# Kernel optimization log

Measured on AMD Instinct MI355X. Metric: run time of the kernel, lower is better.

## Reference

```python
import jax, jax.numpy as jnp
import numpy as np

N = 50000       # nodes
E = 800000      # edges (before self-loops)
F_IN = 256      # input feature dim
HID = 32        # hidden per head
HEADS = 4
CLASSES = 32


def setup_inputs() -> dict:
    key = jax.random.key(0)
    ks = jax.random.split(key, 10)
    x = jax.random.normal(ks[0], (N, F_IN), dtype=jnp.float32)
    edge_index = jax.random.randint(ks[1], (2, E), 0, N, dtype=jnp.int32)
    s1 = 1.0 / np.sqrt(F_IN)
    s2 = 1.0 / np.sqrt(HEADS * HID)
    W1 = jax.random.normal(ks[2], (HEADS * HID, F_IN), dtype=jnp.float32) * s1
    a_src1 = jax.random.normal(ks[3], (HEADS, HID), dtype=jnp.float32) * 0.1
    a_dst1 = jax.random.normal(ks[4], (HEADS, HID), dtype=jnp.float32) * 0.1
    b1 = jnp.zeros((HEADS * HID,), dtype=jnp.float32)
    W2 = jax.random.normal(ks[5], (CLASSES, HEADS * HID), dtype=jnp.float32) * s2
    a_src2 = jax.random.normal(ks[6], (1, CLASSES), dtype=jnp.float32) * 0.1
    a_dst2 = jax.random.normal(ks[7], (1, CLASSES), dtype=jnp.float32) * 0.1
    b2 = jnp.zeros((CLASSES,), dtype=jnp.float32)
    return {"x": x, "edge_index": edge_index,
            "W1": W1, "a_src1": a_src1, "a_dst1": a_dst1, "b1": b1,
            "W2": W2, "a_src2": a_src2, "a_dst2": a_dst2, "b2": b2}


def gat_conv(x, src, dst, W, a_src, a_dst, b, heads, ch):
    """PyG GATConv: linear -> per-head additive attention -> segment softmax over dst -> scatter-sum."""
    n = x.shape[0]
    h = (x @ W.T).reshape(n, heads, ch)                      # [N,H,C]
    asc = jnp.einsum('nhc,hc->nh', h, a_src)                 # att_src . h_j
    adc = jnp.einsum('nhc,hc->nh', h, a_dst)                 # att_dst . h_i
    e = jax.nn.leaky_relu(asc[src] + adc[dst], 0.2)          # [E,H]
    m = jax.ops.segment_max(e, dst, num_segments=n)          # stable softmax per destination
    p = jnp.exp(e - m[dst])
    denom = jax.ops.segment_sum(p, dst, num_segments=n)
    alpha = p / (denom[dst] + 1e-16)                         # [E,H]
    out = jax.ops.segment_sum(h[src] * alpha[:, :, None], dst, num_segments=n)  # [N,H,C]
    return out.reshape(n, heads * ch) + b


def reference(x, edge_index, W1, a_src1, a_dst1, b1, W2, a_src2, a_dst2, b2):
    # PyG GATConv default add_self_loops=True
    loops = jnp.arange(N, dtype=edge_index.dtype)
    src = jnp.concatenate([edge_index[0], loops])
    dst = jnp.concatenate([edge_index[1], loops])
    h = gat_conv(x, src, dst, W1, a_src1, a_dst1, b1, HEADS, HID)
    h = jax.nn.relu(h)                                       # dropout is identity in eval mode
    out = gat_conv(h, src, dst, W2, a_src2, a_dst2, b2, 1, CLASSES)
    return jax.nn.log_softmax(out, axis=1)
```

## Files before the change

kernel.cpp:

```cpp
#include <hip/hip_runtime.h>
#include <hip/hip_fp16.h>

#define N_NODES 50000
#define E_EDGES 800000
#define ET (E_EDGES + N_NODES)
#define NBKT 1024
#define BCAP 2048
#define SCAP 2112
#define CSTR 16
#define G1_BLOCKS 391
#define P_BLOCKS 250
#define P_EPB 3200

typedef _Float16 h8 __attribute__((ext_vector_type(8)));
typedef float f32x16 __attribute__((ext_vector_type(16)));

__device__ __forceinline__ float lrelu(float v) { return v > 0.f ? v : 0.2f * v; }

__global__ __launch_bounds__(256) void prep_kernel(const float* __restrict__ W1,
                                                   const float* __restrict__ W2,
                                                   const float* __restrict__ as1,
                                                   const float* __restrict__ ad1,
                                                   _Float16* __restrict__ w1h,
                                                   _Float16* __restrict__ w2h,
                                                   int* __restrict__ cursor) {
    int i = blockIdx.x * 256 + threadIdx.x;
    if (i < NBKT * CSTR) {
        cursor[i] = 0;
    } else if (i < NBKT * CSTR + 4096) {
        int j = (i - NBKT * CSTR) * 8;
#pragma unroll
        for (int t = 0; t < 8; t++) w1h[j + t] = (_Float16)W1[j + t];
    } else if (i < NBKT * CSTR + 4608) {
        int j = (i - (NBKT * CSTR + 4096)) * 8;
#pragma unroll
        for (int t = 0; t < 8; t++) w2h[j + t] = (_Float16)W2[j + t];
    } else if (i < NBKT * CSTR + 5376) {
        int j = (i - (NBKT * CSTR + 4608)) * 8;
#pragma unroll
        for (int t = 0; t < 8; t++) w1h[136 * 256 + j + t] = (_Float16)0.f;
    } else if (i < NBKT * CSTR + 7424) {
        int a = i - (NBKT * CSTR + 5376);
        int h = a >> 8, k = a & 255;
        const float* av = (h < 4 ? as1 : ad1) + (h & 3) * 32;
        const float* wb = W1 + (size_t)(h & 3) * 32 * 256 + k;
        float s = 0.f;
#pragma unroll
        for (int c = 0; c < 32; c++) s += av[c] * wb[(size_t)c * 256];
        w1h[(size_t)(128 + h) * 256 + k] = (_Float16)s;
    }
}

__global__ __launch_bounds__(256) void gp_kernel(const float* __restrict__ x,
                                                 const int* __restrict__ ei,
                                                 const _Float16* __restrict__ w1h,
                                                 _Float16* __restrict__ h1h,
                                                 float* __restrict__ asc1,
                                                 float* __restrict__ adc1,
                                                 int* __restrict__ cursor,
                                                 int* __restrict__ scratch) {
    __shared__ int hcnt[NBKT];
    __shared__ int hbase[NBKT];
    int tid = threadIdx.x;
    if (blockIdx.x >= G1_BLOCKS) {
        int b = blockIdx.x - G1_BLOCKS;
#pragma unroll
        for (int u = 0; u < NBKT / 256; u++) hcnt[u * 256 + tid] = 0;
        __syncthreads();
        int e0 = b * P_EPB;
        const int4* s4 = (const int4*)(ei + e0);
        const int4* d4 = (const int4*)(ei + E_EDGES + e0);
        for (int q = tid; q < P_EPB / 4; q += 256) {
            int4 d = d4[q];
            atomicAdd(&hcnt[d.x >> 6], 1);
            atomicAdd(&hcnt[d.y >> 6], 1);
            atomicAdd(&hcnt[d.z >> 6], 1);
            atomicAdd(&hcnt[d.w >> 6], 1);
        }
        __syncthreads();
        int rot = (b * 197) & (NBKT - 1);
#pragma unroll
        for (int u = 0; u < NBKT / 256; u++) {
            int bb = (u * 256 + tid + rot) & (NBKT - 1);
            int c = hcnt[bb];
            hbase[bb] = (c > 0) ? atomicAdd(&cursor[bb * CSTR], c) : 0;
            hcnt[bb] = 0;
        }
        __syncthreads();
        for (int q = tid; q < P_EPB / 4; q += 256) {
            int4 s = s4[q];
            int4 d = d4[q];
            int bk, pos;
            bk = d.x >> 6; pos = hbase[bk] + atomicAdd(&hcnt[bk], 1);
            scratch[(size_t)bk * BCAP + pos] = s.x | ((d.x & 63) << 16);
            bk = d.y >> 6; pos = hbase[bk] + atomicAdd(&hcnt[bk], 1);
            scratch[(size_t)bk * BCAP + pos] = s.y | ((d.y & 63) << 16);
            bk = d.z >> 6; pos = hbase[bk] + atomicAdd(&hcnt[bk], 1);
            scratch[(size_t)bk * BCAP + pos] = s.z | ((d.z & 63) << 16);
            bk = d.w >> 6; pos = hbase[bk] + atomicAdd(&hcnt[bk], 1);
            scratch[(size_t)bk * BCAP + pos] = s.w | ((d.w & 63) << 16);
        }
        return;
    }
    int wid = tid >> 6, lane = tid & 63;
    int rbase = blockIdx.x * 128 + wid * 32;
    if (rbase >= N_NODES) return;
    int l31 = lane & 31, l5 = lane >> 5;
    int ar = rbase + l31;
    if (ar > N_NODES - 1) ar = N_NODES - 1;
    const float* ap = x + (size_t)ar * 256 + l5 * 8;
    const _Float16* bp = w1h + (size_t)l31 * 256 + l5 * 8;
    f32x16 acc0 = {}, acc1 = {}, acc2 = {}, acc3 = {}, acc4 = {};
#pragma unroll 4
    for (int ks = 0; ks < 16; ks++) {
        float4 xa = *(const float4*)(ap + ks * 16);
        float4 xb = *(const float4*)(ap + ks * 16 + 4);
        h8 av;
        av[0] = (_Float16)xa.x; av[1] = (_Float16)xa.y;
        av[2] = (_Float16)xa.z; av[3] = (_Float16)xa.w;
        av[4] = (_Float16)xb.x; av[5] = (_Float16)xb.y;
        av[6] = (_Float16)xb.z; av[7] = (_Float16)xb.w;
        h8 b0 = *(const h8*)(bp + ks * 16);
        h8 b1 = *(const h8*)(bp + 32 * 256 + ks * 16);
        h8 b2 = *(const h8*)(bp + 64 * 256 + ks * 16);
        h8 b3 = *(const h8*)(bp + 96 * 256 + ks * 16);
        h8 b4 = *(const h8*)(bp + 128 * 256 + ks * 16);
        acc0 = __builtin_amdgcn_mfma_f32_32x32x16_f16(av, b0, acc0, 0, 0, 0);
        acc1 = __builtin_amdgcn_mfma_f32_32x32x16_f16(av, b1, acc1, 0, 0, 0);
        acc2 = __builtin_amdgcn_mfma_f32_32x32x16_f16(av, b2, acc2, 0, 0, 0);
        acc3 = __builtin_amdgcn_mfma_f32_32x32x16_f16(av, b3, acc3, 0, 0, 0);
        acc4 = __builtin_amdgcn_mfma_f32_32x32x16_f16(av, b4, acc4, 0, 0, 0);
    }
#pragma unroll
    for (int j = 0; j < 16; j++) {
        int row = rbase + (j & 3) + 8 * (j >> 2) + 4 * l5;
        if (row < N_NODES) {
            h1h[(size_t)row * 128 + 0  + l31] = (_Float16)acc0[j];
            h1h[(size_t)row * 128 + 32 + l31] = (_Float16)acc1[j];
            h1h[(size_t)row * 128 + 64 + l31] = (_Float16)acc2[j];
            h1h[(size_t)row * 128 + 96 + l31] = (_Float16)acc3[j];
            float v4 = acc4[j];
            if (l31 < 4) asc1[(size_t)row * 4 + l31] = v4;
            else if (l31 < 8) adc1[(size_t)row * 4 + (l31 - 4)] = v4;
        }
    }
}

__global__ __launch_bounds__(512) void fa_kernel(const int* __restrict__ scratch,
                                                 const int* __restrict__ cursor,
                                                 const float* __restrict__ asc1,
                                                 const float* __restrict__ adc1,
                                                 const __half* __restrict__ h1h,
                                                 const float* __restrict__ b1,
                                                 int* __restrict__ off,
                                                 int* __restrict__ srcs,
                                                 __half* __restrict__ h1b) {
    __shared__ int rec[BCAP];
    __shared__ int ssrc[SCAP];
    __shared__ int sp01[SCAP];
    __shared__ int sp23[SCAP];
    __shared__ int fh[64];
    __shared__ int fcur[64];
    __shared__ int lstart[64];
    __shared__ int red[512];
    int b = blockIdx.x;
    int tid = threadIdx.x;
    int cnt = cursor[b * CSTR];
    int part = 0;
    for (int i = tid; i < b; i += 512) part += cursor[i * CSTR];
    red[tid] = part;
    if (tid < 64) fh[tid] = 0;
    __syncthreads();
    for (int s = 256; s >= 1; s >>= 1) {
        if (tid < s) red[tid] += red[tid + s];
        __syncthreads();
    }
    int gbase = red[0] + b * 64;
    for (int k = tid; k < cnt; k += 512) {
        int r = scratch[(size_t)b * BCAP + k];
        rec[k] = r;
        atomicAdd(&fh[r >> 16], 1);
    }
    __syncthreads();
    if (tid < 64) {
        int n = b * 64 + tid;
        int v = fh[tid] + ((n < N_NODES) ? 1 : 0);
        int incl = v;
#pragma unroll
        for (int d = 1; d < 64; d <<= 1) {
            int u = __shfl_up(incl, d);
            if (tid >= d) incl += u;
        }
        int excl = incl - v;
        lstart[tid] = excl;
        fcur[tid] = excl + ((n < N_NODES) ? 1 : 0);
        if (n < N_NODES) off[n] = gbase + excl;
    }
    if (b == 781 && tid == 0) off[N_NODES] = ET;
    __syncthreads();
    if (tid < 64) {
        int n = b * 64 + tid;
        if (n < N_NODES) {
            int pos = lstart[tid];
            float4 av = *(const float4*)(asc1 + (size_t)n * 4);
            float4 dv = *(const float4*)(adc1 + (size_t)n * 4);
            __half2 p01 = __floats2half2_rn(__expf(lrelu(av.x + dv.x)), __expf(lrelu(av.y + dv.y)));
            __half2 p23 = __floats2half2_rn(__expf(lrelu(av.z + dv.z)), __expf(lrelu(av.w + dv.w)));
            ssrc[pos] = n;
            sp01[pos] = *(int*)&p01;
            sp23[pos] = *(int*)&p23;
            srcs[gbase + pos] = n;
        }
    }
    for (int k = tid; k < cnt; k += 512) {
        int r = rec[k];
        int src = r & 0xFFFF;
        int fbin = r >> 16;
        int dst = b * 64 + fbin;
        int pos = atomicAdd(&fcur[fbin], 1);
        float4 av = *(const float4*)(asc1 + (size_t)src * 4);
        float4 dv = *(const float4*)(adc1 + (size_t)dst * 4);
        __half2 p01 = __floats2half2_rn(__expf(lrelu(av.x + dv.x)), __expf(lrelu(av.y + dv.y)));
        __half2 p23 = __floats2half2_rn(__expf(lrelu(av.z + dv.z)), __expf(lrelu(av.w + dv.w)));
        ssrc[pos] = src;
        sp01[pos] = *(int*)&p01;
        sp23[pos] = *(int*)&p23;
        srcs[gbase + pos] = src;
    }
    __syncthreads();
    int wid = tid >> 6, lane = tid & 63;
    int hh = lane >> 4;
    const __half2* h1h2 = (const __half2*)h1h;
    float bl0 = b1[2 * lane], bl1 = b1[2 * lane + 1];
    for (int ln = wid * 8; ln < wid * 8 + 8; ln++) {
        int node = b * 64 + ln;
        if (node >= N_NODES) break;
        int s0l = lstart[ln];
        int s1l = fcur[ln];
        float den = 0.f, a0 = 0.f, a1 = 0.f;
        int j = s0l;
        for (; j + 8 <= s1l; j += 8) {
            int src8[8];
            int pv[8];
#pragma unroll
            for (int u = 0; u < 8; u++) {
                src8[u] = ssrc[j + u];
                pv[u] = (hh & 2) ? sp23[j + u] : sp01[j + u];
            }
            __half2 hv[8];
#pragma unroll
            for (int u = 0; u < 8; u++) hv[u] = h1h2[(size_t)src8[u] * 64 + lane];
#pragma unroll
            for (int u = 0; u < 8; u++) {
                union { int u32; __half2 h; } v;
                v.u32 = pv[u];
                float p = __half2float((hh & 1) ? v.h.y : v.h.x);
                float2 f = __half22float2(hv[u]);
                den += p;
                a0 += p * f.x;
                a1 += p * f.y;
            }
        }
        for (; j + 4 <= s1l; j += 4) {
            int src4[4];
            int pv[4];
#pragma unroll
            for (int u = 0; u < 4; u++) {
                src4[u] = ssrc[j + u];
                pv[u] = (hh & 2) ? sp23[j + u] : sp01[j + u];
            }
            __half2 hv[4];
#pragma unroll
            for (int u = 0; u < 4; u++) hv[u] = h1h2[(size_t)src4[u] * 64 + lane];
#pragma unroll
            for (int u = 0; u < 4; u++) {
                union { int u32; __half2 h; } v;
                v.u32 = pv[u];
                float p = __half2float((hh & 1) ? v.h.y : v.h.x);
                float2 f = __half22float2(hv[u]);
                den += p;
                a0 += p * f.x;
                a1 += p * f.y;
            }
        }
        for (; j < s1l; j++) {
            union { int u32; __half2 h; } v;
            v.u32 = (hh & 2) ? sp23[j] : sp01[j];
            float p = __half2float((hh & 1) ? v.h.y : v.h.x);
            float2 f = __half22float2(h1h2[(size_t)ssrc[j] * 64 + lane]);
            den += p;
            a0 += p * f.x;
            a1 += p * f.y;
        }
        float inv = 1.f / (den + 1e-16f);
        float o0 = fmaxf(a0 * inv + bl0, 0.f);
        float o1 = fmaxf(a1 * inv + bl1, 0.f);
        ((__half2*)h1b)[(size_t)node * 64 + lane] = __floats2half2_rn(o0, o1);
    }
}

__global__ __launch_bounds__(256) void gemm2_mfma(const __half* __restrict__ h1b,
                                                  const _Float16* __restrict__ w2h,
                                                  const float* __restrict__ as2,
                                                  const float* __restrict__ ad2,
                                                  __half* __restrict__ h2h,
                                                  float* __restrict__ asc2,
                                                  float* __restrict__ adc2) {
    int wid = threadIdx.x >> 6, lane = threadIdx.x & 63;
    int rbase = blockIdx.x * 128 + wid * 32;
    if (rbase >= N_NODES) return;
    int l31 = lane & 31, l5 = lane >> 5;
    int ar = rbase + l31;
    if (ar > N_NODES - 1) ar = N_NODES - 1;
    const _Float16* ap = (const _Float16*)h1b + (size_t)ar * 128 + l5 * 8;
    const _Float16* bp = w2h + (size_t)l31 * 128 + l5 * 8;
    f32x16 acc = {};
#pragma unroll
    for (int ks = 0; ks < 8; ks++) {
        h8 av = *(const h8*)(ap + ks * 16);
        h8 bv = *(const h8*)(bp + ks * 16);
        acc = __builtin_amdgcn_mfma_f32_32x32x16_f16(av, bv, acc, 0, 0, 0);
    }
    float asw = as2[l31], adw = ad2[l31];
#pragma unroll
    for (int j = 0; j < 16; j++) {
        int row = rbase + (j & 3) + 8 * (j >> 2) + 4 * l5;
        float v = acc[j];
        float sv = v * asw, dv = v * adw;
#pragma unroll
        for (int m = 1; m <= 16; m <<= 1) {
            sv += __shfl_xor(sv, m);
            dv += __shfl_xor(dv, m);
        }
        if (row < N_NODES) {
            h2h[(size_t)row * 32 + l31] = __float2half(v);
            if (l31 == 0) { asc2[row] = sv; adc2[row] = dv; }
        }
    }
}

__global__ __launch_bounds__(256) void agg2_kernel(const __half* __restrict__ h2h,
                                                   const int* __restrict__ srcs,
                                                   const float* __restrict__ asc2,
                                                   const float* __restrict__ adc2,
                                                   const float* __restrict__ b2,
                                                   const int* __restrict__ off,
                                                   float* __restrict__ out) {
    int wid = threadIdx.x >> 6, lane = threadIdx.x & 63;
    int node = blockIdx.x * 4 + wid;
    if (node >= N_NODES) return;
    int g = lane >> 4;
    int li = lane & 15;
    const __half2* h2h2 = (const __half2*)h2h;
    float adv = adc2[node];
    int s0 = off[node], s1 = off[node + 1];
    float den = 0.f, a0 = 0.f, a1 = 0.f;
    int j = s0 + g;
    for (; j + 16 <= s1; j += 16) {
        int s[4];
#pragma unroll
        for (int u = 0; u < 4; u++) s[u] = srcs[j + 4 * u];
        float av[4];
#pragma unroll
        for (int u = 0; u < 4; u++) av[u] = asc2[s[u]];
        __half2 hv[4];
#pragma unroll
        for (int u = 0; u < 4; u++) hv[u] = h2h2[(size_t)s[u] * 16 + li];
#pragma unroll
        for (int u = 0; u < 4; u++) {
            float p = __expf(lrelu(av[u] + adv));
            float2 f = __half22float2(hv[u]);
            den += p;
            a0 += p * f.x;
            a1 += p * f.y;
        }
    }
    for (; j < s1; j += 4) {
        int s = srcs[j];
        float p = __expf(lrelu(asc2[s] + adv));
        float2 f = __half22float2(h2h2[(size_t)s * 16 + li]);
        den += p;
        a0 += p * f.x;
        a1 += p * f.y;
    }
    den += __shfl_xor(den, 16); den += __shfl_xor(den, 32);
    a0 += __shfl_xor(a0, 16);  a0 += __shfl_xor(a0, 32);
    a1 += __shfl_xor(a1, 16);  a1 += __shfl_xor(a1, 32);
    float inv = 1.f / (den + 1e-16f);
    float v0 = a0 * inv + b2[2 * li];
    float v1 = a1 * inv + b2[2 * li + 1];
    float mx = fmaxf(v0, v1);
#pragma unroll
    for (int msk = 8; msk >= 1; msk >>= 1) mx = fmaxf(mx, __shfl_xor(mx, msk));
    float se = __expf(v0 - mx) + __expf(v1 - mx);
#pragma unroll
    for (int msk = 8; msk >= 1; msk >>= 1) se += __shfl_xor(se, msk);
    float lse = mx + __logf(se);
    if (lane < 16) {
        ((float2*)out)[(size_t)node * 16 + li] = make_float2(v0 - lse, v1 - lse);
    }
}

extern "C" void kernel_launch(void* const* d_in, const int* in_sizes, int n_in,
                              void* d_out, int out_size, void* d_ws, size_t ws_size,
                              hipStream_t stream) {
    const float* x   = (const float*)d_in[0];
    const int* ei    = (const int*)d_in[1];
    const float* W1  = (const float*)d_in[2];
    const float* as1 = (const float*)d_in[3];
    const float* ad1 = (const float*)d_in[4];
    const float* b1  = (const float*)d_in[5];
    const float* W2  = (const float*)d_in[6];
    const float* as2 = (const float*)d_in[7];
    const float* ad2 = (const float*)d_in[8];
    const float* b2  = (const float*)d_in[9];
    float* out = (float*)d_out;

    char* base = (char*)d_ws;
    int* cursor   = (int*)base;
    int* scratch  = (int*)(base + 13600000);
    _Float16* w1h = (_Float16*)(base + 30377216);
    _Float16* w2h = (_Float16*)(base + 30459136);
    _Float16* h1h = (_Float16*)(base + 30467328);
    __half* h1b   = (__half*)(base + 43267328);
    __half* h2h   = (__half*)(base + 56067328);
    float* asc1   = (float*)(base + 59267328);
    float* adc1   = (float*)(base + 60067328);
    float* asc2   = (float*)(base + 60867328);
    float* adc2   = (float*)(base + 61067328);
    int* off      = (int*)(base + 61267328);
    int* srcs     = (int*)(base + 61471428);

    prep_kernel<<<93, 256, 0, stream>>>(W1, W2, as1, ad1, w1h, w2h, cursor);
    gp_kernel<<<G1_BLOCKS + P_BLOCKS, 256, 0, stream>>>(x, ei, w1h, h1h, asc1, adc1, cursor, scratch);
    fa_kernel<<<782, 512, 0, stream>>>(scratch, cursor, asc1, adc1, (const __half*)h1h, b1, off, srcs, h1b);
    gemm2_mfma<<<391, 256, 0, stream>>>(h1b, w2h, as2, ad2, h2h, asc2, adc2);
    agg2_kernel<<<(N_NODES + 3) / 4, 256, 0, stream>>>(h2h, srcs, asc2, adc2, b2, off, out);
}
```

Baseline: 122.5 us.

## Fuse layer-2 GEMM into layer-1 aggregation kernel via shared-memory tile

The layer-1 aggregation output for each 64-node block is now kept in a 16 KB shared-memory tile rather than written to global memory. Four waves then run the layer-2 MFMA GEMM directly from that tile. The attention vectors a_src2/a_dst2 are folded into extra rows of an extended W2 matrix in the prep kernel, so asc2 and adc2 come out of the GEMM instead of a shuffle reduction. This removes one kernel launch and the global round trip of h1b, at the cost of extra LDS pressure in fa_kernel, which may lower occupancy.

```diff
diff --git a/kernel.cpp b/kernel.cpp
--- a/kernel.cpp
+++ b/kernel.cpp
@@ -11,6 +11,7 @@
 #define G1_BLOCKS 391
 #define P_BLOCKS 250
 #define P_EPB 3200
+#define PB0 (NBKT * CSTR)
 
 typedef _Float16 h8 __attribute__((ext_vector_type(8)));
 typedef float f32x16 __attribute__((ext_vector_type(16)));
@@ -21,26 +22,28 @@
                                                    const float* __restrict__ W2,
                                                    const float* __restrict__ as1,
                                                    const float* __restrict__ ad1,
+                                                   const float* __restrict__ as2,
+                                                   const float* __restrict__ ad2,
                                                    _Float16* __restrict__ w1h,
-                                                   _Float16* __restrict__ w2h,
+                                                   _Float16* __restrict__ w2e,
                                                    int* __restrict__ cursor) {
     int i = blockIdx.x * 256 + threadIdx.x;
-    if (i < NBKT * CSTR) {
+    if (i < PB0) {
         cursor[i] = 0;
-    } else if (i < NBKT * CSTR + 4096) {
-        int j = (i - NBKT * CSTR) * 8;
+    } else if (i < PB0 + 4096) {
+        int j = (i - PB0) * 8;
 #pragma unroll
         for (int t = 0; t < 8; t++) w1h[j + t] = (_Float16)W1[j + t];
-    } else if (i < NBKT * CSTR + 4608) {
-        int j = (i - (NBKT * CSTR + 4096)) * 8;
-#pragma unroll
-        for (int t = 0; t < 8; t++) w2h[j + t] = (_Float16)W2[j + t];
-    } else if (i < NBKT * CSTR + 5376) {
-        int j = (i - (NBKT * CSTR + 4608)) * 8;
+    } else if (i < PB0 + 4608) {
+        int j = (i - (PB0 + 4096)) * 8;
+#pragma unroll
+        for (int t = 0; t < 8; t++) w2e[j + t] = (_Float16)W2[j + t];
+    } else if (i < PB0 + 5376) {
+        int j = (i - (PB0 + 4608)) * 8;
 #pragma unroll
         for (int t = 0; t < 8; t++) w1h[136 * 256 + j + t] = (_Float16)0.f;
-    } else if (i < NBKT * CSTR + 7424) {
-        int a = i - (NBKT * CSTR + 5376);
+    } else if (i < PB0 + 7424) {
+        int a = i - (PB0 + 5376);
         int h = a >> 8, k = a & 255;
         const float* av = (h < 4 ? as1 : ad1) + (h & 3) * 32;
         const float* wb = W1 + (size_t)(h & 3) * 32 * 256 + k;
@@ -48,6 +51,17 @@
 #pragma unroll
         for (int c = 0; c < 32; c++) s += av[c] * wb[(size_t)c * 256];
         w1h[(size_t)(128 + h) * 256 + k] = (_Float16)s;
+    } else if (i < PB0 + 7680) {
+        int a = i - (PB0 + 7424);
+        int h = a >> 7, k = a & 127;
+        const float* av = h ? ad2 : as2;
+        float s = 0.f;
+#pragma unroll
+        for (int c = 0; c < 32; c++) s += av[c] * W2[(size_t)c * 128 + k];
+        w2e[(size_t)(32 + h) * 128 + k] = (_Float16)s;
+    } else if (i < PB0 + 8160) {
+        int j = (i - (PB0 + 7680)) * 8;
+        for (int t = 0; t < 8; t++) w2e[34 * 128 + j + t] = (_Float16)0.f;
     }
 }
 
@@ -152,9 +166,12 @@
                                                  const float* __restrict__ adc1,
                                                  const __half* __restrict__ h1h,
                                                  const float* __restrict__ b1,
+                                                 const _Float16* __restrict__ w2e,
                                                  int* __restrict__ off,
                                                  int* __restrict__ srcs,
-                                                 __half* __restrict__ h1b) {
+                                                 __half* __restrict__ h2h,
+                                                 float* __restrict__ asc2,
+                                                 float* __restrict__ adc2) {
     __shared__ int rec[BCAP];
     __shared__ int ssrc[SCAP];
     __shared__ int sp01[SCAP];
@@ -163,6 +180,7 @@
     __shared__ int fcur[64];
     __shared__ int lstart[64];
     __shared__ int red[512];
+    __shared__ _Float16 h1t[64 * 128];
     int b = blockIdx.x;
     int tid = threadIdx.x;
     int cnt = cursor[b * CSTR];
@@ -232,9 +250,13 @@
     int hh = lane >> 4;
     const __half2* h1h2 = (const __half2*)h1h;
     float bl0 = b1[2 * lane], bl1 = b1[2 * lane + 1];
+    __half2* h1t2 = (__half2*)h1t;
     for (int ln = wid * 8; ln < wid * 8 + 8; ln++) {
         int node = b * 64 + ln;
-        if (node >= N_NODES) break;
+        if (node >= N_NODES) {
+            h1t2[ln * 64 + lane] = __floats2half2_rn(0.f, 0.f);
+            continue;
+        }
         int s0l = lstart[ln];
         int s1l = fcur[ln];
         float den = 0.f, a0 = 0.f, a1 = 0.f;
@@ -295,46 +317,35 @@
         float inv = 1.f / (den + 1e-16f);
         float o0 = fmaxf(a0 * inv + bl0, 0.f);
         float o1 = fmaxf(a1 * inv + bl1, 0.f);
-        ((__half2*)h1b)[(size_t)node * 64 + lane] = __floats2half2_rn(o0, o1);
-    }
-}
-
-__global__ __launch_bounds__(256) void gemm2_mfma(const __half* __restrict__ h1b,
-                                                  const _Float16* __restrict__ w2h,
-                                                  const float* __restrict__ as2,
-                                                  const float* __restrict__ ad2,
-                                                  __half* __restrict__ h2h,
-                                                  float* __restrict__ asc2,
-                                                  float* __restrict__ adc2) {
-    int wid = threadIdx.x >> 6, lane = threadIdx.x & 63;
-    int rbase = blockIdx.x * 128 + wid * 32;
-    if (rbase >= N_NODES) return;
-    int l31 = lane & 31, l5 = lane >> 5;
-    int ar = rbase + l31;
-    if (ar > N_NODES - 1) ar = N_NODES - 1;
-    const _Float16* ap = (const _Float16*)h1b + (size_t)ar * 128 + l5 * 8;
-    const _Float16* bp = w2h + (size_t)l31 * 128 + l5 * 8;
-    f32x16 acc = {};
-#pragma unroll
-    for (int ks = 0; ks < 8; ks++) {
-        h8 av = *(const h8*)(ap + ks * 16);
-        h8 bv = *(const h8*)(bp + ks * 16);
-        acc = __builtin_amdgcn_mfma_f32_32x32x16_f16(av, bv, acc, 0, 0, 0);
-    }
-    float asw = as2[l31], adw = ad2[l31];
-#pragma unroll
-    for (int j = 0; j < 16; j++) {
-        int row = rbase + (j & 3) + 8 * (j >> 2) + 4 * l5;
-        float v = acc[j];
-        float sv = v * asw, dv = v * adw;
-#pragma unroll
-        for (int m = 1; m <= 16; m <<= 1) {
-            sv += __shfl_xor(sv, m);
-            dv += __shfl_xor(dv, m);
-        }
-        if (row < N_NODES) {
-            h2h[(size_t)row * 32 + l31] = __float2half(v);
-            if (l31 == 0) { asc2[row] = sv; adc2[row] = dv; }
+        h1t2[ln * 64 + lane] = __floats2half2_rn(o0, o1);
+    }
+    __syncthreads();
+    if (wid < 4) {
+        int tr = wid >> 1;
+        int tc = wid & 1;
+        int l31 = lane & 31, l5 = lane >> 5;
+        const _Float16* ap = h1t + (size_t)(tr * 32 + l31) * 128 + l5 * 8;
+        const _Float16* bp = w2e + (size_t)(tc * 32 + l31) * 128 + l5 * 8;
+        f32x16 acc = {};
+#pragma unroll
+        for (int ks = 0; ks < 8; ks++) {
+            h8 av = *(const h8*)(ap + ks * 16);
+            h8 bv = *(const h8*)(bp + ks * 16);
+            acc = __builtin_amdgcn_mfma_f32_32x32x16_f16(av, bv, acc, 0, 0, 0);
+        }
+#pragma unroll
+        for (int j = 0; j < 16; j++) {
+            int row = tr * 32 + (j & 3) + 8 * (j >> 2) + 4 * l5;
+            int node = b * 64 + row;
+            if (node < N_NODES) {
+                float v = acc[j];
+                if (tc == 0) {
+                    h2h[(size_t)node * 32 + l31] = __float2half(v);
+                } else {
+                    if (l31 == 0) asc2[node] = v;
+                    else if (l31 == 1) adc2[node] = v;
+                }
+            }
         }
     }
 }
@@ -420,9 +431,8 @@
     int* cursor   = (int*)base;
     int* scratch  = (int*)(base + 13600000);
     _Float16* w1h = (_Float16*)(base + 30377216);
-    _Float16* w2h = (_Float16*)(base + 30459136);
     _Float16* h1h = (_Float16*)(base + 30467328);
-    __half* h1b   = (__half*)(base + 43267328);
+    _Float16* w2e = (_Float16*)(base + 43267328);
     __half* h2h   = (__half*)(base + 56067328);
     float* asc1   = (float*)(base + 59267328);
     float* adc1   = (float*)(base + 60067328);
@@ -431,9 +441,9 @@
     int* off      = (int*)(base + 61267328);
     int* srcs     = (int*)(base + 61471428);
 
-    prep_kernel<<<93, 256, 0, stream>>>(W1, W2, as1, ad1, w1h, w2h, cursor);
+    prep_kernel<<<(PB0 + 8160 + 255) / 256, 256, 0, stream>>>(W1, W2, as1, ad1, as2, ad2, w1h, w2e, cursor);
     gp_kernel<<<G1_BLOCKS + P_BLOCKS, 256, 0, stream>>>(x, ei, w1h, h1h, asc1, adc1, cursor, scratch);
-    fa_kernel<<<782, 512, 0, stream>>>(scratch, cursor, asc1, adc1, (const __half*)h1h, b1, off, srcs, h1b);
-    gemm2_mfma<<<391, 256, 0, stream>>>(h1b, w2h, as2, ad2, h2h, asc2, adc2);
+    fa_kernel<<<782, 512, 0, stream>>>(scratch, cursor, asc1, adc1, (const __half*)h1h, b1, w2e,
+                                       off, srcs, h2h, asc2, adc2);
     agg2_kernel<<<(N_NODES + 3) / 4, 256, 0, stream>>>(h2h, srcs, asc2, adc2, b2, off, out);
 }
```

Result: no change. 124.5 us (+1.6%).
